# Performance work log

Measured on AMD Instinct MI355X. Metric: run time of the kernel, lower is better.

## Reference

```python
import jax, jax.numpy as jnp
import numpy as np

B, L, D, H = 2, 1024, 1024, 16
HD = D // H
HIDDEN = 4 * D
EPS = 1e-6
SCALE = HD ** -0.5

# RoPE tables (head_dim is even, so rope_dim == head_dim)
_inv_freq = 1.0 / (10000.0 ** (np.arange(0, HD, 2, dtype=np.float32) / HD))
_freqs = np.arange(L, dtype=np.float32)[:, None] * _inv_freq[None, :]          # [L, HD/2]
COS = jnp.asarray(np.concatenate([np.cos(_freqs), np.cos(_freqs)], -1))        # [L, HD]
SIN = jnp.asarray(np.concatenate([np.sin(_freqs), np.sin(_freqs)], -1))
MASK = jnp.tril(jnp.ones((L, L), dtype=bool))                                   # causal


def _clin(xr, xi, Wr, Wi, br=None, bi=None):
    # complex linear: (a+bi)(c+di), weights stored [out, in] as in torch
    r = xr @ Wr.T - xi @ Wi.T
    i = xr @ Wi.T + xi @ Wr.T
    if br is not None:
        r = r + br
        i = i + bi
    return r, i


def _cln(xr, xi, gr, gi, br, bi):
    mr = xr.mean(-1, keepdims=True)
    mi = xi.mean(-1, keepdims=True)
    cr = xr - mr
    ci = xi - mi
    var = (cr * cr + ci * ci).mean(-1, keepdims=True)
    s = jnp.sqrt(var + EPS)
    nr = cr / s
    ni = ci / s
    return nr * gr - ni * gi + br, nr * gi + ni * gr + bi


def _rot_half(x):
    h = x.shape[-1] // 2
    return jnp.concatenate([-x[..., h:], x[..., :h]], -1)


def _rope(xr, xi):
    # apply same real rotation to real and imag parts (matches torch code)
    return (xr * COS + _rot_half(xr) * SIN, xi * COS + _rot_half(xi) * SIN)


def _split_heads(x):
    return x.reshape(B, L, H, HD).transpose(0, 2, 1, 3)  # [B,H,L,HD]


def _merge_heads(x):
    return x.transpose(0, 2, 1, 3).reshape(B, L, D)


def setup_inputs() -> dict:
    key = jax.random.key(0)
    ks = jax.random.split(key, 20)
    n = lambda k, shape, s=1.0: jax.random.normal(k, shape, dtype=jnp.float32) * s
    s_attn = (2.0 * (D + D)) ** -0.5
    s_fc1 = (2.0 * (D + HIDDEN)) ** -0.5
    s_fc2 = (2.0 * (HIDDEN + D)) ** -0.5
    return {
        'x_real': n(ks[0], (B, L, D)),
        'x_imag': n(ks[1], (B, L, D)),
        'Wq_r': n(ks[2], (D, D), s_attn), 'Wq_i': n(ks[3], (D, D), s_attn),
        'Wk_r': n(ks[4], (D, D), s_attn), 'Wk_i': n(ks[5], (D, D), s_attn),
        'Wv_r': n(ks[6], (D, D), s_attn), 'Wv_i': n(ks[7], (D, D), s_attn),
        'Wo_r': n(ks[8], (D, D), s_attn), 'Wo_i': n(ks[9], (D, D), s_attn),
        'bo_r': jnp.zeros((D,), jnp.float32), 'bo_i': jnp.zeros((D,), jnp.float32),
        'ln1_gr': jnp.ones((D,), jnp.float32), 'ln1_gi': jnp.zeros((D,), jnp.float32),
        'ln1_br': jnp.zeros((D,), jnp.float32), 'ln1_bi': jnp.zeros((D,), jnp.float32),
        'ln2_gr': jnp.ones((D,), jnp.float32), 'ln2_gi': jnp.zeros((D,), jnp.float32),
        'ln2_br': jnp.zeros((D,), jnp.float32), 'ln2_bi': jnp.zeros((D,), jnp.float32),
        'W1_r': n(ks[10], (HIDDEN, D), s_fc1), 'W1_i': n(ks[11], (HIDDEN, D), s_fc1),
        'b1_r': jnp.zeros((HIDDEN,), jnp.float32), 'b1_i': jnp.zeros((HIDDEN,), jnp.float32),
        'W2_r': n(ks[12], (D, HIDDEN), s_fc2), 'W2_i': n(ks[13], (D, HIDDEN), s_fc2),
        'b2_r': jnp.zeros((D,), jnp.float32), 'b2_i': jnp.zeros((D,), jnp.float32),
        'mod_b': n(ks[14], (HIDDEN,), 0.1),
    }


def reference(x_real, x_imag,
              Wq_r, Wq_i, Wk_r, Wk_i, Wv_r, Wv_i, Wo_r, Wo_i, bo_r, bo_i,
              ln1_gr, ln1_gi, ln1_br, ln1_bi, ln2_gr, ln2_gi, ln2_br, ln2_bi,
              W1_r, W1_i, b1_r, b1_i, W2_r, W2_i, b2_r, b2_i, mod_b):
    # --- attention sublayer (pre-LN) ---
    hr, hi = _cln(x_real, x_imag, ln1_gr, ln1_gi, ln1_br, ln1_bi)
    Qr, Qi = _clin(hr, hi, Wq_r, Wq_i)
    Kr, Ki = _clin(hr, hi, Wk_r, Wk_i)
    Vr, Vi = _clin(hr, hi, Wv_r, Wv_i)
    Qr, Qi, Kr, Ki = map(_split_heads, (Qr, Qi, Kr, Ki))
    Vr, Vi = _split_heads(Vr), _split_heads(Vi)
    Qr, Qi = _rope(Qr, Qi)
    Kr, Ki = _rope(Kr, Ki)
    # Hermitian inner product real part: Re(Q K*) = Qr.Kr + Qi.Ki
    scores = (jnp.einsum('bhld,bhmd->bhlm', Qr, Kr)
              + jnp.einsum('bhld,bhmd->bhlm', Qi, Ki)) * SCALE
    scores = jnp.where(MASK, scores, -jnp.inf)
    attn = jax.nn.softmax(scores, axis=-1)
    out_r = _merge_heads(jnp.einsum('bhlm,bhmd->bhld', attn, Vr))
    out_i = _merge_heads(jnp.einsum('bhlm,bhmd->bhld', attn, Vi))
    out_r, out_i = _clin(out_r, out_i, Wo_r, Wo_i, bo_r, bo_i)
    ar = x_real + out_r
    ai = x_imag + out_i
    # --- feed-forward sublayer (pre-LN) ---
    hr, hi = _cln(ar, ai, ln2_gr, ln2_gi, ln2_br, ln2_bi)
    fr, fi = _clin(hr, hi, W1_r, W1_i, b1_r, b1_i)
    # ModReLU: relu(|z| + b) * e^{i angle(z)}
    mag = jnp.sqrt(fr * fr + fi * fi)
    safe = jnp.where(mag > 0, mag, 1.0)
    act = jax.nn.relu(mag + mod_b)
    fr, fi = act * fr / safe, act * fi / safe
    fr, fi = _clin(fr, fi, W2_r, W2_i, b2_r, b2_i)
    return ar + fr, ai + fi
```

## Files before the change

kernel.cpp:

```cpp
#include <hip/hip_runtime.h>

#define Bq 2
#define Lq 1024
#define Dq 1024
#define Hq 16
#define HDq 64
#define HIDq 4096
#define Mq (Bq*Lq)

typedef __bf16 bf16x8 __attribute__((ext_vector_type(8)));
typedef float floatx4 __attribute__((ext_vector_type(4)));
typedef float floatx16 __attribute__((ext_vector_type(16)));

__device__ __forceinline__ unsigned short f2us(float f){
  unsigned u = __builtin_bit_cast(unsigned, f);
  u = u + 0x7fffu + ((u >> 16) & 1u);
  return (unsigned short)(u >> 16);
}

__device__ __forceinline__ void gld16(const unsigned short* g, unsigned short* l){
  __builtin_amdgcn_global_load_lds(
      (const __attribute__((address_space(1))) unsigned int*)g,
      (__attribute__((address_space(3))) unsigned int*)l, 16, 0, 0);
}

__global__ __launch_bounds__(256) void cvt4_kernel(
    const float* __restrict__ s0, const float* __restrict__ s1,
    const float* __restrict__ s2, const float* __restrict__ s3,
    unsigned short* __restrict__ d0, unsigned short* __restrict__ d1,
    unsigned short* __restrict__ d2, unsigned short* __restrict__ d3,
    int n)
{
  const int a = blockIdx.y;
  const float* s = (a==0) ? s0 : (a==1) ? s1 : (a==2) ? s2 : s3;
  unsigned short* d = (a==0) ? d0 : (a==1) ? d1 : (a==2) ? d2 : d3;
  const int i = (blockIdx.x * 256 + threadIdx.x) * 8;
  if (i >= n) return;
  float4 v0 = ((const float4*)(s + i))[0];
  float4 v1 = ((const float4*)(s + i))[1];
  ushort4 o0, o1;
  o0.x=f2us(v0.x); o0.y=f2us(v0.y); o0.z=f2us(v0.z); o0.w=f2us(v0.w);
  o1.x=f2us(v1.x); o1.y=f2us(v1.y); o1.z=f2us(v1.z); o1.w=f2us(v1.w);
  ((ushort4*)(d + i))[0] = o0;
  ((ushort4*)(d + i))[1] = o1;
}

__global__ __launch_bounds__(256) void cln_kernel(
    const float* __restrict__ xr, const float* __restrict__ xi,
    const float* __restrict__ gr, const float* __restrict__ gi,
    const float* __restrict__ br, const float* __restrict__ bi,
    unsigned short* __restrict__ outr, unsigned short* __restrict__ outi)
{
  const int row = blockIdx.x;
  const int t = threadIdx.x;
  const int lane = t & 63, wv = t >> 6;
  __shared__ float sred[8];

  float4 v4r = ((const float4*)(xr + (size_t)row*Dq))[t];
  float4 v4i = ((const float4*)(xi + (size_t)row*Dq))[t];
  float vr[4] = {v4r.x, v4r.y, v4r.z, v4r.w};
  float vi[4] = {v4i.x, v4i.y, v4i.z, v4i.w};
  float sr = vr[0]+vr[1]+vr[2]+vr[3];
  float si = vi[0]+vi[1]+vi[2]+vi[3];
  #pragma unroll
  for (int o=32;o>0;o>>=1){ sr += __shfl_down(sr,o,64); si += __shfl_down(si,o,64); }
  if (lane==0){ sred[wv]=sr; sred[4+wv]=si; }
  __syncthreads();
  float mr = (sred[0]+sred[1]+sred[2]+sred[3]) * (1.0f/Dq);
  float mi = (sred[4]+sred[5]+sred[6]+sred[7]) * (1.0f/Dq);
  float cr[4], ci[4], vs = 0.f;
  #pragma unroll
  for (int j=0;j<4;++j){ cr[j]=vr[j]-mr; ci[j]=vi[j]-mi; vs += cr[j]*cr[j]+ci[j]*ci[j]; }
  #pragma unroll
  for (int o=32;o>0;o>>=1) vs += __shfl_down(vs,o,64);
  __syncthreads();
  if (lane==0) sred[wv]=vs;
  __syncthreads();
  float var = (sred[0]+sred[1]+sred[2]+sred[3]) * (1.0f/Dq);
  float inv = rsqrtf(var + 1e-6f);

  float4 g4r = ((const float4*)gr)[t];
  float4 g4i = ((const float4*)gi)[t];
  float4 b4r = ((const float4*)br)[t];
  float4 b4i = ((const float4*)bi)[t];
  float grf[4] = {g4r.x,g4r.y,g4r.z,g4r.w};
  float gif[4] = {g4i.x,g4i.y,g4i.z,g4i.w};
  float brf[4] = {b4r.x,b4r.y,b4r.z,b4r.w};
  float bif[4] = {b4i.x,b4i.y,b4i.z,b4i.w};
  ushort4 o_r, o_i;
  unsigned short orr[4], oii[4];
  #pragma unroll
  for (int j=0;j<4;++j){
    float nr = cr[j]*inv, ni = ci[j]*inv;
    orr[j] = f2us(nr*grf[j] - ni*gif[j] + brf[j]);
    oii[j] = f2us(nr*gif[j] + ni*grf[j] + bif[j]);
  }
  o_r.x=orr[0]; o_r.y=orr[1]; o_r.z=orr[2]; o_r.w=orr[3];
  o_i.x=oii[0]; o_i.y=oii[1]; o_i.z=oii[2]; o_i.w=oii[3];
  ((ushort4*)(outr + (size_t)row*Dq))[t] = o_r;
  ((ushort4*)(outi + (size_t)row*Dq))[t] = o_i;
}

template<int EPI, bool ROPE, bool SPLIT3>
__global__ __launch_bounds__(128,2) void cgemm32_kernel(
    const unsigned short* __restrict__ Ar, const unsigned short* __restrict__ Ai,
    const unsigned short* __restrict__ Wr, const unsigned short* __restrict__ Wi,
    void* __restrict__ Cr0, void* __restrict__ Ci0,
    void* __restrict__ Cr1, void* __restrict__ Ci1,
    void* __restrict__ Cr2, void* __restrict__ Ci2,
    const float* __restrict__ biasR, const float* __restrict__ biasI,
    const float* __restrict__ resR, const float* __restrict__ resI,
    const float* __restrict__ modb,
    int Ndim, int Kdim)
{
  const int t = threadIdx.x;
  const int w = t >> 6, l = t & 63;
  const int l31 = l & 31, lhi = l >> 5;
  const int m0 = blockIdx.x * 64, n0 = blockIdx.y * 64;

  __shared__ __align__(16) unsigned short sAr[64*64], sAi[64*64], sWr[64*64], sWi[64*64];

  floatx16 accRR[2], accII[2], accRI[2], accIR[2];
  #pragma unroll
  for (int i=0;i<2;++i){
    #pragma unroll
    for (int r=0;r<16;++r){ accRR[i][r]=0.f; accII[i][r]=0.f; accRI[i][r]=0.f; accIR[i][r]=0.f; }
  }

  const int srow = t >> 3;
  const int lc = (((t & 7) ^ ((t >> 3) & 7))) * 8;
  const unsigned short* pAr = Ar + (size_t)(m0 + srow)*Kdim + lc;
  const unsigned short* pAi = Ai + (size_t)(m0 + srow)*Kdim + lc;
  const unsigned short* pWr = Wr + (size_t)(n0 + srow)*Kdim + lc;
  const unsigned short* pWi = Wi + (size_t)(n0 + srow)*Kdim + lc;
  const int dst0 = t * 8;

  const int arow = w*32 + l31;
  int aoff[4], woff0[4], woff1[4];
  #pragma unroll
  for (int kh=0; kh<4; ++kh){
    const int c = kh*2 + lhi;
    aoff[kh]  = arow*64      + ((c ^ (arow & 7)) * 8);
    woff0[kh] = l31*64       + ((c ^ (l31 & 7)) * 8);
    woff1[kh] = (32+l31)*64  + ((c ^ (l31 & 7)) * 8);
  }

  const int nk = Kdim >> 6;
  for (int kk=0; kk<nk; ++kk){
    #pragma unroll
    for (int j=0;j<4;++j){
      const size_t so = (size_t)j * 16 * Kdim;
      gld16(pAr + so, &sAr[dst0 + j*1024]);
      gld16(pAi + so, &sAi[dst0 + j*1024]);
      gld16(pWr + so, &sWr[dst0 + j*1024]);
      gld16(pWi + so, &sWi[dst0 + j*1024]);
    }
    pAr += 64; pAi += 64; pWr += 64; pWi += 64;
    __syncthreads();
    #pragma unroll
    for (int kh=0; kh<4; ++kh){
      bf16x8 fAr  = *(const bf16x8*)&sAr[aoff[kh]];
      bf16x8 fAi  = *(const bf16x8*)&sAi[aoff[kh]];
      bf16x8 fW0r = *(const bf16x8*)&sWr[woff0[kh]];
      bf16x8 fW0i = *(const bf16x8*)&sWi[woff0[kh]];
      bf16x8 fW1r = *(const bf16x8*)&sWr[woff1[kh]];
      bf16x8 fW1i = *(const bf16x8*)&sWi[woff1[kh]];
      accRR[0] = __builtin_amdgcn_mfma_f32_32x32x16_bf16(fAr, fW0r, accRR[0], 0,0,0);
      accII[0] = __builtin_amdgcn_mfma_f32_32x32x16_bf16(fAi, fW0i, accII[0], 0,0,0);
      accRI[0] = __builtin_amdgcn_mfma_f32_32x32x16_bf16(fAr, fW0i, accRI[0], 0,0,0);
      accIR[0] = __builtin_amdgcn_mfma_f32_32x32x16_bf16(fAi, fW0r, accIR[0], 0,0,0);
      accRR[1] = __builtin_amdgcn_mfma_f32_32x32x16_bf16(fAr, fW1r, accRR[1], 0,0,0);
      accII[1] = __builtin_amdgcn_mfma_f32_32x32x16_bf16(fAi, fW1i, accII[1], 0,0,0);
      accRI[1] = __builtin_amdgcn_mfma_f32_32x32x16_bf16(fAr, fW1i, accRI[1], 0,0,0);
      accIR[1] = __builtin_amdgcn_mfma_f32_32x32x16_bf16(fAi, fW1r, accIR[1], 0,0,0);
    }
    __syncthreads();
  }

  float cr[2][16], ci[2][16];
  #pragma unroll
  for (int nf=0; nf<2; ++nf)
    #pragma unroll
    for (int r=0;r<16;++r){
      cr[nf][r] = accRR[nf][r] - accII[nf][r];
      ci[nf][r] = accRI[nf][r] + accIR[nf][r];
    }

  const bool doRope = ROPE && (!SPLIT3 || (n0 < 2048));
  if (doRope){
    const float invf = powf(10000.0f, -(float)l31 * (1.0f/32.0f));
    #pragma unroll
    for (int r=0;r<16;++r){
      const int gm = m0 + w*32 + (r&3) + 8*(r>>2) + 4*lhi;
      float s, c;
      sincosf((float)(gm & (Lq-1)) * invf, &s, &c);
      float xr_ = cr[0][r], yr_ = cr[1][r];
      cr[0][r] = xr_*c - yr_*s;  cr[1][r] = yr_*c + xr_*s;
      float xi_ = ci[0][r], yi_ = ci[1][r];
      ci[0][r] = xi_*c - yi_*s;  ci[1][r] = yi_*c + xi_*s;
    }
  }

  unsigned short *oR16 = nullptr, *oI16 = nullptr;
  float *oR32 = nullptr, *oI32 = nullptr;
  int ncol0, Nst;
  if (SPLIT3){
    const int aid = n0 >> 10;
    void* vr = (aid==0) ? Cr0 : ((aid==1) ? Cr1 : Cr2);
    void* vi = (aid==0) ? Ci0 : ((aid==1) ? Ci1 : Ci2);
    oR16 = (unsigned short*)vr; oI16 = (unsigned short*)vi;
    ncol0 = n0 & 1023; Nst = 1024;
  } else {
    oR16 = (unsigned short*)Cr0; oI16 = (unsigned short*)Ci0;
    oR32 = (float*)Cr0;          oI32 = (float*)Ci0;
    ncol0 = n0; Nst = Ndim;
  }

  #pragma unroll
  for (int nf=0; nf<2; ++nf){
    const int gn = n0 + nf*32 + l31;
    const int cn = ncol0 + nf*32 + l31;
    float bR = 0.f, bI = 0.f, mb = 0.f;
    if (EPI >= 1){ bR = biasR[gn]; bI = biasI[gn]; }
    if (EPI == 2){ mb = modb[gn]; }
    #pragma unroll
    for (int r=0;r<16;++r){
      const int gm = m0 + w*32 + (r&3) + 8*(r>>2) + 4*lhi;
      const size_t idx = (size_t)gm*Nst + cn;
      float vr_ = cr[nf][r] + bR, vi_ = ci[nf][r] + bI;
      if (EPI == 1 || EPI == 3){ vr_ += resR[idx]; vi_ += resI[idx]; }
      if (EPI == 2){
        float mag = sqrtf(vr_*vr_ + vi_*vi_);
        float safe = (mag > 0.f) ? mag : 1.0f;
        float act = fmaxf(mag + mb, 0.f);
        float sc = act / safe;
        vr_ *= sc; vi_ *= sc;
      }
      if (EPI == 0 || EPI == 2){
        oR16[idx] = f2us(vr_);
        oI16[idx] = f2us(vi_);
      } else {
        oR32[idx] = vr_;
        oI32[idx] = vi_;
      }
    }
  }
}

__global__ __launch_bounds__(256) void vtrans_kernel(
    const unsigned short* __restrict__ Vr, const unsigned short* __restrict__ Vi,
    unsigned short* __restrict__ VTr, unsigned short* __restrict__ VTi)
{
  const int lt = blockIdx.x;
  const int bh = blockIdx.y;
  const int h = bh & (Hq-1), b = bh >> 4;
  const int t = threadIdx.x;
  __shared__ unsigned short sTr[64*65], sTi[64*65];

  const int row = t >> 2;
  const int dc  = (t & 3) * 16;
  const size_t g = ((size_t)(b*Lq) + lt*64 + row)*Dq + h*HDq + dc;
  uint4 a0 = *(const uint4*)(Vr + g);
  uint4 a1 = *(const uint4*)(Vr + g + 8);
  uint4 b0 = *(const uint4*)(Vi + g);
  uint4 b1 = *(const uint4*)(Vi + g + 8);
  const unsigned short* pa0 = (const unsigned short*)&a0;
  const unsigned short* pa1 = (const unsigned short*)&a1;
  const unsigned short* pb0 = (const unsigned short*)&b0;
  const unsigned short* pb1 = (const unsigned short*)&b1;
  #pragma unroll
  for (int e=0;e<8;++e){
    sTr[(dc+e)*65 + row]   = pa0[e];
    sTr[(dc+8+e)*65 + row] = pa1[e];
    sTi[(dc+e)*65 + row]   = pb0[e];
    sTi[(dc+8+e)*65 + row] = pb1[e];
  }
  __syncthreads();
  const int d  = t >> 2;
  const int lcx = (t & 3) * 16;
  unsigned short bufr[16], bufi[16];
  #pragma unroll
  for (int e=0;e<16;++e){
    bufr[e] = sTr[d*65 + lcx + e];
    bufi[e] = sTi[d*65 + lcx + e];
  }
  const size_t og = ((size_t)bh*HDq + d)*Lq + lt*64 + lcx;
  *(uint4*)(VTr + og)     = *(const uint4*)&bufr[0];
  *(uint4*)(VTr + og + 8) = *(const uint4*)&bufr[8];
  *(uint4*)(VTi + og)     = *(const uint4*)&bufi[0];
  *(uint4*)(VTi + og + 8) = *(const uint4*)&bufi[8];
}

__device__ __forceinline__ int swz(int v){ return v ^ ((v >> 4) & 7); }

__global__ __launch_bounds__(256,2) void fattn_kernel(
    const unsigned short* __restrict__ Qr, const unsigned short* __restrict__ Qi,
    const unsigned short* __restrict__ Kr, const unsigned short* __restrict__ Ki,
    const unsigned short* __restrict__ VTr, const unsigned short* __restrict__ VTi,
    unsigned short* __restrict__ Or, unsigned short* __restrict__ Oi)
{
  const int qt = (int)(gridDim.x - 1 - blockIdx.x);
  const int bh = blockIdx.y;
  const int h = bh & (Hq-1), b = bh >> 4;
  const int t = threadIdx.x;
  const int w = t >> 6, lane = t & 63;
  const int quad = lane >> 4, l15 = lane & 15;

  __shared__ __align__(16) unsigned short sKr[4096], sKi[4096], sVr[4096], sVi[4096];
  __shared__ __align__(16) unsigned short sP[64*72];

  const size_t qbase = ((size_t)(b*Lq) + qt*64 + w*16 + l15)*Dq + h*HDq;
  bf16x8 qr_lo = *(const bf16x8*)(Qr + qbase + quad*8);
  bf16x8 qr_hi = *(const bf16x8*)(Qr + qbase + 32 + quad*8);
  bf16x8 qi_lo = *(const bf16x8*)(Qi + qbase + quad*8);
  bf16x8 qi_hi = *(const bf16x8*)(Qi + qbase + 32 + quad*8);

  const floatx4 fzero = {0.f,0.f,0.f,0.f};
  floatx4 aOr[4], aOi[4];
  #pragma unroll
  for (int i=0;i<4;++i){ aOr[i]=fzero; aOi[i]=fzero; }
  float m_run[4] = {-1e30f,-1e30f,-1e30f,-1e30f};
  float l_run[4] = {0.f,0.f,0.f,0.f};

  const int srow = t >> 2;
  const int sns  = srow >> 4;
  const int sl15 = srow & 15;
  const int q8   = (t & 3) * 2;
  const int dstA = sns*1024 + swz(q8*16 + sl15)*8;
  const int dstB = sns*1024 + swz((q8+1)*16 + sl15)*8;

  const int rd0 = swz(quad*16 + l15)*8;
  const int rd1 = swz((4+quad)*16 + l15)*8;

  for (int kt = 0; kt <= qt; ++kt){
    const size_t kg = ((size_t)(b*Lq) + kt*64 + srow)*Dq + h*HDq + q8*8;
    uint4 ka = *(const uint4*)(Kr + kg);
    uint4 kb = *(const uint4*)(Kr + kg + 8);
    uint4 kc = *(const uint4*)(Ki + kg);
    uint4 kd = *(const uint4*)(Ki + kg + 8);
    const size_t vg = ((size_t)bh*HDq + srow)*Lq + kt*64 + q8*8;
    uint4 va = *(const uint4*)(VTr + vg);
    uint4 vb = *(const uint4*)(VTr + vg + 8);
    uint4 vc = *(const uint4*)(VTi + vg);
    uint4 vd = *(const uint4*)(VTi + vg + 8);
    __syncthreads();
    *(uint4*)&sKr[dstA] = ka;  *(uint4*)&sKr[dstB] = kb;
    *(uint4*)&sKi[dstA] = kc;  *(uint4*)&sKi[dstB] = kd;
    *(uint4*)&sVr[dstA] = va;  *(uint4*)&sVr[dstB] = vb;
    *(uint4*)&sVi[dstA] = vc;  *(uint4*)&sVi[dstB] = vd;
    __syncthreads();

    floatx4 sc[4];
    #pragma unroll
    for (int ns=0; ns<4; ++ns){
      floatx4 x = fzero;
      x = __builtin_amdgcn_mfma_f32_16x16x32_bf16(qr_lo, *(const bf16x8*)&sKr[ns*1024 + rd0], x, 0,0,0);
      x = __builtin_amdgcn_mfma_f32_16x16x32_bf16(qr_hi, *(const bf16x8*)&sKr[ns*1024 + rd1], x, 0,0,0);
      x = __builtin_amdgcn_mfma_f32_16x16x32_bf16(qi_lo, *(const bf16x8*)&sKi[ns*1024 + rd0], x, 0,0,0);
      x = __builtin_amdgcn_mfma_f32_16x16x32_bf16(qi_hi, *(const bf16x8*)&sKi[ns*1024 + rd1], x, 0,0,0);
      sc[ns] = x;
    }

    const bool diag = (kt == qt);
    float rmax[4] = {-1e30f,-1e30f,-1e30f,-1e30f};
    #pragma unroll
    for (int ns=0; ns<4; ++ns){
      #pragma unroll
      for (int r=0; r<4; ++r){
        float s = sc[ns][r] * 0.125f;
        if (diag && (ns*16 + l15 > w*16 + quad*4 + r)) s = -1e30f;
        sc[ns][r] = s;
        rmax[r] = fmaxf(rmax[r], s);
      }
    }
    #pragma unroll
    for (int off=1; off<16; off<<=1){
      #pragma unroll
      for (int r=0; r<4; ++r) rmax[r] = fmaxf(rmax[r], __shfl_xor(rmax[r], off, 64));
    }

    float alpha[4], rsum[4];
    #pragma unroll
    for (int r=0; r<4; ++r){
      float mn = fmaxf(m_run[r], rmax[r]);
      alpha[r] = __expf(m_run[r] - mn);
      m_run[r] = mn;
      rsum[r] = 0.f;
    }
    #pragma unroll
    for (int ns=0; ns<4; ++ns){
      #pragma unroll
      for (int r=0; r<4; ++r){
        float p = __expf(sc[ns][r] - m_run[r]);
        rsum[r] += p;
        sP[(w*16 + quad*4 + r)*72 + ns*16 + l15] = f2us(p);
      }
    }
    #pragma unroll
    for (int off=1; off<16; off<<=1){
      #pragma unroll
      for (int r=0; r<4; ++r) rsum[r] += __shfl_xor(rsum[r], off, 64);
    }
    #pragma unroll
    for (int r=0; r<4; ++r) l_run[r] = l_run[r]*alpha[r] + rsum[r];
    #pragma unroll
    for (int ds=0; ds<4; ++ds)
      #pragma unroll
      for (int r=0; r<4; ++r){ aOr[ds][r] *= alpha[r]; aOi[ds][r] *= alpha[r]; }

    #pragma unroll
    for (int step=0; step<2; ++step){
      bf16x8 pf = *(const bf16x8*)&sP[(w*16 + l15)*72 + step*32 + quad*8];
      const int ro = (step==0) ? rd0 : rd1;
      #pragma unroll
      for (int ds=0; ds<4; ++ds){
        aOr[ds] = __builtin_amdgcn_mfma_f32_16x16x32_bf16(pf, *(const bf16x8*)&sVr[ds*1024 + ro], aOr[ds], 0,0,0);
        aOi[ds] = __builtin_amdgcn_mfma_f32_16x16x32_bf16(pf, *(const bf16x8*)&sVi[ds*1024 + ro], aOi[ds], 0,0,0);
      }
    }
  }

  #pragma unroll
  for (int r=0; r<4; ++r){
    const float il = 1.0f / l_run[r];
    const size_t ob = ((size_t)(b*Lq) + qt*64 + w*16 + quad*4 + r)*Dq + h*HDq;
    #pragma unroll
    for (int ds=0; ds<4; ++ds){
      Or[ob + ds*16 + l15] = f2us(aOr[ds][r] * il);
      Oi[ob + ds*16 + l15] = f2us(aOi[ds][r] * il);
    }
  }
}

extern "C" void kernel_launch(void* const* d_in, const int* in_sizes, int n_in,
                              void* d_out, int out_size, void* d_ws, size_t ws_size,
                              hipStream_t stream)
{
  const float* x_r    = (const float*)d_in[0];
  const float* x_i    = (const float*)d_in[1];
  const float* Wq_r   = (const float*)d_in[2];
  const float* Wq_i   = (const float*)d_in[3];
  const float* Wk_r   = (const float*)d_in[4];
  const float* Wk_i   = (const float*)d_in[5];
  const float* Wv_r   = (const float*)d_in[6];
  const float* Wv_i   = (const float*)d_in[7];
  const float* Wo_r   = (const float*)d_in[8];
  const float* Wo_i   = (const float*)d_in[9];
  const float* bo_r   = (const float*)d_in[10];
  const float* bo_i   = (const float*)d_in[11];
  const float* ln1_gr = (const float*)d_in[12];
  const float* ln1_gi = (const float*)d_in[13];
  const float* ln1_br = (const float*)d_in[14];
  const float* ln1_bi = (const float*)d_in[15];
  const float* ln2_gr = (const float*)d_in[16];
  const float* ln2_gi = (const float*)d_in[17];
  const float* ln2_br = (const float*)d_in[18];
  const float* ln2_bi = (const float*)d_in[19];
  const float* W1_r   = (const float*)d_in[20];
  const float* W1_i   = (const float*)d_in[21];
  const float* b1_r   = (const float*)d_in[22];
  const float* b1_i   = (const float*)d_in[23];
  const float* W2_r   = (const float*)d_in[24];
  const float* W2_i   = (const float*)d_in[25];
  const float* b2_r   = (const float*)d_in[26];
  const float* b2_i   = (const float*)d_in[27];
  const float* mod_b  = (const float*)d_in[28];

  char* wsb = (char*)d_ws;
  const size_t MB = 1024*1024;
  unsigned short* bQKV_r = (unsigned short*)(wsb + 0*MB);
  unsigned short* bQKV_i = (unsigned short*)(wsb + 6*MB);
  unsigned short* bWo_r = (unsigned short*)(wsb + 12*MB);
  unsigned short* bWo_i = (unsigned short*)(wsb + 14*MB);
  unsigned short* bW1_r = (unsigned short*)(wsb + 16*MB);
  unsigned short* bW1_i = (unsigned short*)(wsb + 24*MB);
  unsigned short* bW2_r = (unsigned short*)(wsb + 32*MB);
  unsigned short* bW2_i = (unsigned short*)(wsb + 40*MB);
  unsigned short* hr  = (unsigned short*)(wsb + 48*MB);
  unsigned short* hi_ = (unsigned short*)(wsb + 52*MB);
  unsigned short* Qr  = (unsigned short*)(wsb + 56*MB);
  unsigned short* Qi  = (unsigned short*)(wsb + 60*MB);
  unsigned short* Kr  = (unsigned short*)(wsb + 64*MB);
  unsigned short* Ki  = (unsigned short*)(wsb + 68*MB);
  unsigned short* Vr  = (unsigned short*)(wsb + 72*MB);
  unsigned short* Vi  = (unsigned short*)(wsb + 76*MB);
  unsigned short* VTr = (unsigned short*)(wsb + 80*MB);
  unsigned short* VTi = (unsigned short*)(wsb + 84*MB);
  unsigned short* Or  = hr;
  unsigned short* Oi  = hi_;
  unsigned short* h2r = Qr;
  unsigned short* h2i = Qi;
  unsigned short* fr  = (unsigned short*)(wsb + 64*MB);
  unsigned short* fi  = (unsigned short*)(wsb + 80*MB);

  float* outR = (float*)d_out;
  float* outI = outR + (size_t)Mq*Dq;

  const dim3 blk(256);
  const dim3 blk128(128);

  const int nDD = Dq*Dq;
  const int nDH = Dq*HIDq;
  cvt4_kernel<<<dim3(nDD/2048, 4), blk, 0, stream>>>(Wq_r, Wk_r, Wv_r, Wo_r,
      bQKV_r, bQKV_r + (size_t)nDD, bQKV_r + (size_t)2*nDD, bWo_r, nDD);
  cvt4_kernel<<<dim3(nDD/2048, 4), blk, 0, stream>>>(Wq_i, Wk_i, Wv_i, Wo_i,
      bQKV_i, bQKV_i + (size_t)nDD, bQKV_i + (size_t)2*nDD, bWo_i, nDD);
  cvt4_kernel<<<dim3(nDH/2048, 4), blk, 0, stream>>>(W1_r, W1_i, W2_r, W2_i,
      bW1_r, bW1_i, bW2_r, bW2_i, nDH);

  cln_kernel<<<Mq, blk, 0, stream>>>(x_r, x_i, ln1_gr, ln1_gi, ln1_br, ln1_bi, hr, hi_);
  cgemm32_kernel<0,true,true><<<dim3(Mq/64, 3072/64), blk128, 0, stream>>>(
      hr, hi_, bQKV_r, bQKV_i,
      Qr, Qi, Kr, Ki, Vr, Vi,
      nullptr, nullptr, nullptr, nullptr, nullptr, 3072, Dq);
  vtrans_kernel<<<dim3(16, 32), blk, 0, stream>>>(Vr, Vi, VTr, VTi);
  fattn_kernel<<<dim3(16, 32), blk, 0, stream>>>(Qr, Qi, Kr, Ki, VTr, VTi, Or, Oi);
  cgemm32_kernel<1,false,false><<<dim3(Mq/64, Dq/64), blk128, 0, stream>>>(
      Or, Oi, bWo_r, bWo_i, outR, outI, nullptr, nullptr, nullptr, nullptr,
      bo_r, bo_i, x_r, x_i, nullptr, Dq, Dq);
  cln_kernel<<<Mq, blk, 0, stream>>>(outR, outI, ln2_gr, ln2_gi, ln2_br, ln2_bi, h2r, h2i);
  cgemm32_kernel<2,false,false><<<dim3(Mq/64, HIDq/64), blk128, 0, stream>>>(
      h2r, h2i, bW1_r, bW1_i, fr, fi, nullptr, nullptr, nullptr, nullptr,
      b1_r, b1_i, nullptr, nullptr, mod_b, HIDq, Dq);
  cgemm32_kernel<3,false,false><<<dim3(Mq/64, Dq/64), blk128, 0, stream>>>(
      fr, fi, bW2_r, bW2_i, outR, outI, nullptr, nullptr, nullptr, nullptr,
      b2_r, b2_i, outR, outI, nullptr, Dq, HIDq);
}
```

Measured before the change: 550.8 us.

## Double-buffer LDS tiles in complex GEMM to overlap global loads with MFMA

The complex GEMM main loop now uses two sets of shared-memory tiles and issues the async global-to-LDS loads for the next K step before computing on the current one. The goal is to hide global memory latency behind MFMA work instead of stalling at a barrier after each load. In exchange, LDS use per block doubles to 64 KB, which may cut occupancy below the two blocks per CU that the launch bounds ask for. The loop also assumes the K tile count is even. Whether the loads finish in time depends on the barrier waiting for outstanding global_load_lds operations, since there is no explicit vmcnt wait.

```diff
diff --git a/kernel.cpp b/kernel.cpp
--- a/kernel.cpp
+++ b/kernel.cpp
@@ -118,7 +118,8 @@
   const int l31 = l & 31, lhi = l >> 5;
   const int m0 = blockIdx.x * 64, n0 = blockIdx.y * 64;
 
-  __shared__ __align__(16) unsigned short sAr[64*64], sAi[64*64], sWr[64*64], sWi[64*64];
+  __shared__ __align__(16) unsigned short sAr0[64*64], sAi0[64*64], sWr0[64*64], sWi0[64*64];
+  __shared__ __align__(16) unsigned short sAr1[64*64], sAi1[64*64], sWr1[64*64], sWi1[64*64];
 
   floatx16 accRR[2], accII[2], accRI[2], accIR[2];
   #pragma unroll
@@ -145,37 +146,48 @@
     woff1[kh] = (32+l31)*64  + ((c ^ (l31 & 7)) * 8);
   }
 
+#define STAGEK(SA, SB, SC, SD, KOFF) do{                                   \
+    _Pragma("unroll")                                                      \
+    for (int j_=0;j_<4;++j_){                                              \
+      const size_t so_ = (size_t)j_ * 16 * Kdim + (size_t)(KOFF);          \
+      gld16(pAr + so_, &SA[dst0 + j_*1024]);                               \
+      gld16(pAi + so_, &SB[dst0 + j_*1024]);                               \
+      gld16(pWr + so_, &SC[dst0 + j_*1024]);                               \
+      gld16(pWi + so_, &SD[dst0 + j_*1024]);                               \
+    } }while(0)
+
+#define COMPUTEK(SA, SB, SC, SD) do{                                       \
+    _Pragma("unroll")                                                      \
+    for (int kh_=0; kh_<4; ++kh_){                                         \
+      bf16x8 fAr  = *(const bf16x8*)&SA[aoff[kh_]];                        \
+      bf16x8 fAi  = *(const bf16x8*)&SB[aoff[kh_]];                        \
+      bf16x8 fW0r = *(const bf16x8*)&SC[woff0[kh_]];                       \
+      bf16x8 fW0i = *(const bf16x8*)&SD[woff0[kh_]];                       \
+      bf16x8 fW1r = *(const bf16x8*)&SC[woff1[kh_]];                       \
+      bf16x8 fW1i = *(const bf16x8*)&SD[woff1[kh_]];                       \
+      accRR[0] = __builtin_amdgcn_mfma_f32_32x32x16_bf16(fAr, fW0r, accRR[0], 0,0,0); \
+      accII[0] = __builtin_amdgcn_mfma_f32_32x32x16_bf16(fAi, fW0i, accII[0], 0,0,0); \
+      accRI[0] = __builtin_amdgcn_mfma_f32_32x32x16_bf16(fAr, fW0i, accRI[0], 0,0,0); \
+      accIR[0] = __builtin_amdgcn_mfma_f32_32x32x16_bf16(fAi, fW0r, accIR[0], 0,0,0); \
+      accRR[1] = __builtin_amdgcn_mfma_f32_32x32x16_bf16(fAr, fW1r, accRR[1], 0,0,0); \
+      accII[1] = __builtin_amdgcn_mfma_f32_32x32x16_bf16(fAi, fW1i, accII[1], 0,0,0); \
+      accRI[1] = __builtin_amdgcn_mfma_f32_32x32x16_bf16(fAr, fW1i, accRI[1], 0,0,0); \
+      accIR[1] = __builtin_amdgcn_mfma_f32_32x32x16_bf16(fAi, fW1r, accIR[1], 0,0,0); \
+    } }while(0)
+
   const int nk = Kdim >> 6;
-  for (int kk=0; kk<nk; ++kk){
-    #pragma unroll
-    for (int j=0;j<4;++j){
-      const size_t so = (size_t)j * 16 * Kdim;
-      gld16(pAr + so, &sAr[dst0 + j*1024]);
-      gld16(pAi + so, &sAi[dst0 + j*1024]);
-      gld16(pWr + so, &sWr[dst0 + j*1024]);
-      gld16(pWi + so, &sWi[dst0 + j*1024]);
-    }
-    pAr += 64; pAi += 64; pWr += 64; pWi += 64;
+  STAGEK(sAr0, sAi0, sWr0, sWi0, 0);
+  __syncthreads();
+  for (int kk=0; kk<nk; kk+=2){
+    STAGEK(sAr1, sAi1, sWr1, sWi1, (kk+1)*64);
+    COMPUTEK(sAr0, sAi0, sWr0, sWi0);
     __syncthreads();
-    #pragma unroll
-    for (int kh=0; kh<4; ++kh){
-      bf16x8 fAr  = *(const bf16x8*)&sAr[aoff[kh]];
-      bf16x8 fAi  = *(const bf16x8*)&sAi[aoff[kh]];
-      bf16x8 fW0r = *(const bf16x8*)&sWr[woff0[kh]];
-      bf16x8 fW0i = *(const bf16x8*)&sWi[woff0[kh]];
-      bf16x8 fW1r = *(const bf16x8*)&sWr[woff1[kh]];
-      bf16x8 fW1i = *(const bf16x8*)&sWi[woff1[kh]];
-      accRR[0] = __builtin_amdgcn_mfma_f32_32x32x16_bf16(fAr, fW0r, accRR[0], 0,0,0);
-      accII[0] = __builtin_amdgcn_mfma_f32_32x32x16_bf16(fAi, fW0i, accII[0], 0,0,0);
-      accRI[0] = __builtin_amdgcn_mfma_f32_32x32x16_bf16(fAr, fW0i, accRI[0], 0,0,0);
-      accIR[0] = __builtin_amdgcn_mfma_f32_32x32x16_bf16(fAi, fW0r, accIR[0], 0,0,0);
-      accRR[1] = __builtin_amdgcn_mfma_f32_32x32x16_bf16(fAr, fW1r, accRR[1], 0,0,0);
-      accII[1] = __builtin_amdgcn_mfma_f32_32x32x16_bf16(fAi, fW1i, accII[1], 0,0,0);
-      accRI[1] = __builtin_amdgcn_mfma_f32_32x32x16_bf16(fAr, fW1i, accRI[1], 0,0,0);
-      accIR[1] = __builtin_amdgcn_mfma_f32_32x32x16_bf16(fAi, fW1r, accIR[1], 0,0,0);
-    }
+    if (kk+2 < nk) STAGEK(sAr0, sAi0, sWr0, sWi0, (kk+2)*64);
+    COMPUTEK(sAr1, sAi1, sWr1, sWi1);
     __syncthreads();
   }
+#undef STAGEK
+#undef COMPUTEK
 
   float cr[2][16], ci[2][16];
   #pragma unroll
```

Measured after the change: 507.1 us. -7.9%, faster.
